# Kernel tuning notes

Measured on AMD Instinct MI355X. Metric: run time of the kernel, lower is better.

The kernel has to match this reference:

```python
import jax, jax.numpy as jnp
import numpy as np

N_NODES = 100000
N_EDGES = 1600000
N_GRAPHS = 64
FEAT = 64
EMB = 64
HID = 64
VOCAB = 32


def setup_inputs() -> dict:
    key = jax.random.key(0)
    ks = jax.random.split(key, 20)
    w = lambda k, sh: (jax.random.normal(k, sh, jnp.float32) * 0.05)
    x = jax.random.normal(ks[0], (N_NODES, FEAT), jnp.float32)
    edge_index = jax.random.randint(ks[1], (2, N_EDGES), 0, N_NODES, dtype=jnp.int32).astype(jnp.int64)
    batch = jnp.sort(jax.random.randint(ks[2], (N_NODES,), 0, N_GRAPHS, dtype=jnp.int32)).astype(jnp.int64)
    return {
        'x': x, 'edge_index': edge_index, 'batch': batch,
        # RGCN layer 1 (single relation): relation weight, root weight, bias
        'W1': w(ks[3], (FEAT, EMB)), 'root1': w(ks[4], (FEAT, EMB)), 'b1': w(ks[5], (EMB,)),
        # RGCN layer 2
        'W2': w(ks[6], (EMB, HID)), 'root2': w(ks[7], (EMB, HID)), 'b2': w(ks[8], (HID,)),
        # init_h / init_c linear heads
        'Wh': w(ks[9], (HID, HID)), 'bh': w(ks[10], (HID,)),
        'Wc': w(ks[11], (HID, HID)), 'bc': w(ks[12], (HID,)),
        # output layer
        'Wo': w(ks[13], (HID, VOCAB)), 'bo': w(ks[14], (VOCAB,)),
    }


def _rgcn(x, edge_index, W, root, b):
    # PyG RGCNConv with num_relations=1, aggr='mean':
    # out[i] = mean_{j in N(i)} (x[j] @ W) + x[i] @ root + b
    src, dst = edge_index[0], edge_index[1]
    msg = x[src] @ W                                    # [E, out] gather + small GEMM
    agg = jax.ops.segment_sum(msg, dst, num_segments=x.shape[0])
    cnt = jax.ops.segment_sum(jnp.ones((edge_index.shape[1],), x.dtype), dst, num_segments=x.shape[0])
    agg = agg / jnp.maximum(cnt, 1.0)[:, None]
    return agg + x @ root + b


def reference(x, edge_index, batch, W1, root1, b1, W2, root2, b2, Wh, bh, Wc, bc, Wo, bo):
    h = jax.nn.relu(_rgcn(x, edge_index, W1, root1, b1))
    h = jax.nn.relu(_rgcn(h, edge_index, W2, root2, b2))
    # global_mean_pool over graph-assignment vector `batch`
    summ = jax.ops.segment_sum(h, batch, num_segments=N_GRAPHS)
    cnt = jax.ops.segment_sum(jnp.ones((h.shape[0],), h.dtype), batch, num_segments=N_GRAPHS)
    pooled = summ / jnp.maximum(cnt, 1.0)[:, None]      # [G, HID]
    hidden = pooled @ Wh + bh
    cell = pooled @ Wc + bc
    logits = jax.nn.log_softmax(hidden @ Wo + bo, axis=1)
    return (logits, hidden, cell)
```

## Files before the change

kernel.cpp:

```cpp
#include <hip/hip_runtime.h>
#include <hip/hip_bf16.h>


typedef __attribute__((ext_vector_type(8))) short short8;
typedef __attribute__((ext_vector_type(4))) float f32x4;
typedef __attribute__((ext_vector_type(2))) float f32x2;

#define RB 9
#define MAXBINS 256
#define CAP 12288
#define BCAP 14336
#define CHUNK 8192

__device__ inline float bf2f(unsigned short h) {
    return __uint_as_float(((unsigned int)h) << 16);
}
__device__ inline float bflo(unsigned int u) { return __uint_as_float(u << 16); }
__device__ inline float bfhi(unsigned int u) { return __uint_as_float(u & 0xffff0000u); }
__device__ inline unsigned short f2bf(float f) {
    unsigned int u = __float_as_uint(f);
    u = (u + 0x7fffu + ((u >> 16) & 1u)) >> 16;
    return (unsigned short)u;
}

__global__ __launch_bounds__(256) void bin_prep(const int* __restrict__ src,
                                                const int* __restrict__ dst,
                                                unsigned int* __restrict__ coarse,
                                                int* __restrict__ gcur,
                                                int E, int BINS, int nbBin,
                                                const float* __restrict__ W1,
                                                const float* __restrict__ R1,
                                                const float* __restrict__ W2,
                                                const float* __restrict__ R2,
                                                unsigned short* __restrict__ bt) {
    __shared__ int cnt[MAXBINS];
    __shared__ int incl[MAXBINS];
    __shared__ int bstart[MAXBINS];
    __shared__ int bcur[MAXBINS];
    __shared__ int gbase[MAXBINS];
    __shared__ unsigned int stage[CHUNK];
    __shared__ unsigned char binOf[CHUNK];

    const int tid = threadIdx.x;
    if (blockIdx.x >= nbBin) {
        const int layer = blockIdx.x - nbBin;
        const float* W = layer ? W2 : W1;
        const float* R = layer ? R2 : R1;
        unsigned short* o = bt + (size_t)layer * 8192;
        for (int idx = tid; idx < 8192; idx += 256) {
            const int n = idx >> 6, k = idx & 63;
            const float v = (n < 64) ? W[k * 64 + n] : R[k * 64 + (n - 64)];
            o[idx] = f2bf(v);
        }
        return;
    }

    const int chunk0 = blockIdx.x * CHUNK;
    int myS[32], myD[32];
#pragma unroll
    for (int k = 0; k < 32; ++k) {
        const int idx = chunk0 + k * 256 + tid;
        if (idx < E) { myS[k] = src[idx]; myD[k] = dst[idx]; }
        else myD[k] = -1;
    }
    cnt[tid] = 0;
    __syncthreads();
#pragma unroll
    for (int k = 0; k < 32; ++k)
        if (myD[k] >= 0) atomicAdd(&cnt[myD[k] >> RB], 1);
    __syncthreads();
    incl[tid] = cnt[tid];
    __syncthreads();
    for (int off = 1; off < 256; off <<= 1) {
        int t = (tid >= off) ? incl[tid - off] : 0;
        __syncthreads();
        incl[tid] += t;
        __syncthreads();
    }
    bstart[tid] = incl[tid] - cnt[tid];
    bcur[tid] = incl[tid] - cnt[tid];
    __syncthreads();
#pragma unroll
    for (int k = 0; k < 32; ++k) {
        if (myD[k] >= 0) {
            const int b = myD[k] >> RB;
            const int pos = atomicAdd(&bcur[b], 1);
            stage[pos] = (unsigned int)myS[k] | ((unsigned int)(myD[k] & ((1 << RB) - 1)) << 17);
            binOf[pos] = (unsigned char)b;
        }
    }
    __syncthreads();
    if (tid < BINS && cnt[tid] > 0)
        gbase[tid] = tid * CAP + atomicAdd(&gcur[tid], cnt[tid]);
    __syncthreads();
    int total = E - chunk0;
    if (total > CHUNK) total = CHUNK;
    for (int idx = tid; idx < total; idx += 256) {
        const int b = binOf[idx];
        coarse[gbase[b] + (idx - bstart[b])] = stage[idx];
    }
}

__device__ inline void store_xw_fp8(unsigned char* __restrict__ xw8, int rowbase, int q,
                                    int t, int mm, const f32x4& accT) {
#pragma unroll
    for (int r = 0; r < 4; ++r) {
        const float v0 = accT[r];
        const float v1 = __shfl_down(v0, 1);
        const float v2 = __shfl_down(v0, 2);
        const float v3 = __shfl_down(v0, 3);
        if (!(mm & 3)) {
            unsigned int u = (unsigned int)__builtin_amdgcn_cvt_pk_fp8_f32(v0, v1, 0, false);
            u = (unsigned int)__builtin_amdgcn_cvt_pk_fp8_f32(v2, v3, (int)u, true);
            *(unsigned int*)&xw8[(size_t)(rowbase + q * 4 + r) * 64 + t * 16 + mm] = u;
        }
    }
}

__global__ __launch_bounds__(256) void fin_gemm1(const unsigned int* __restrict__ coarse,
                                                 const int* __restrict__ gcur,
                                                 int* __restrict__ bucket,
                                                 int* __restrict__ pstart,
                                                 int* __restrict__ degarr,
                                                 int N, int BINS,
                                                 const float* __restrict__ x,
                                                 const unsigned short* __restrict__ bt,
                                                 const float* __restrict__ bias,
                                                 unsigned char* __restrict__ xw8,
                                                 unsigned short* __restrict__ xrb) {
    __shared__ int ncnt[512];
    __shared__ int pexcl[512];
    __shared__ int ncur[512];
    __shared__ int s2[256];
    __shared__ int ptot;

    const int tid = threadIdx.x;
    if (blockIdx.x < (unsigned)BINS) {
        const int b = blockIdx.x;
        const int cb = gcur[b];
        const int base = b * BCAP;
        const unsigned int* reg = coarse + (size_t)b * CAP;
        const int node0 = b << RB;
        int nloc = N - node0;
        if (nloc > 512) nloc = 512;

        ncnt[tid] = 0; ncnt[tid + 256] = 0;
        __syncthreads();
        for (int idx = tid; idx < cb; idx += 256)
            atomicAdd(&ncnt[reg[idx] >> 17], 1);
        __syncthreads();
        const int p0 = (ncnt[2 * tid] + 15) & ~15;
        const int p1 = (ncnt[2 * tid + 1] + 15) & ~15;
        s2[tid] = p0 + p1;
        __syncthreads();
        for (int off = 1; off < 256; off <<= 1) {
            int t = (tid >= off) ? s2[tid - off] : 0;
            __syncthreads();
            s2[tid] += t;
            __syncthreads();
        }
        const int pairExcl = s2[tid] - (p0 + p1);
        pexcl[2 * tid] = pairExcl;
        pexcl[2 * tid + 1] = pairExcl + p0;
        ncur[2 * tid] = pairExcl;
        ncur[2 * tid + 1] = pairExcl + p0;
        if (tid == 255) ptot = s2[255];
        __syncthreads();
        const int total = ptot;
        for (int i = tid; i < nloc; i += 256) {
            pstart[node0 + i] = base + pexcl[i];
            degarr[node0 + i] = ncnt[i];
        }
        for (int idx = tid; idx < total; idx += 256) bucket[base + idx] = N;
        __syncthreads();
        for (int idx = tid; idx < cb; idx += 256) {
            const unsigned int e = reg[idx];
            const int p = atomicAdd(&ncur[e >> 17], 1);
            bucket[base + p] = (int)(e & 0x1FFFFu);
        }
        return;
    }

    const int gb = blockIdx.x - BINS;
    if (gb == 0 && tid < 16)
        *(unsigned int*)&xw8[(size_t)N * 64 + tid * 4] = 0u;

    const int lane = tid & 63;
    const int q = lane >> 4;
    const int mm = lane & 15;

    short8 bfrag[8][2];
#pragma unroll
    for (int t = 0; t < 8; ++t)
#pragma unroll
        for (int c = 0; c < 2; ++c)
            bfrag[t][c] = *(const short8*)&bt[(size_t)(t * 16 + mm) * 64 + c * 32 + q * 8];
    float bv[4];
#pragma unroll
    for (int tt = 0; tt < 4; ++tt) bv[tt] = bias[tt * 16 + mm];

    const int wid = tid >> 6;
    const int gw = gb * 4 + wid;
    const int nw = 1024 * 4;
    const int ntiles = N >> 4;

    for (int tile = gw; tile < ntiles; tile += nw) {
        const int row0 = tile << 4;
        const float* ap = &x[(size_t)(row0 + mm) * 64 + q * 8];
        const float4 f0 = *(const float4*)ap;
        const float4 f1 = *(const float4*)(ap + 4);
        const float4 f2 = *(const float4*)(ap + 32);
        const float4 f3 = *(const float4*)(ap + 36);
        short8 a0, a1;
        a0[0] = (short)f2bf(f0.x); a0[1] = (short)f2bf(f0.y);
        a0[2] = (short)f2bf(f0.z); a0[3] = (short)f2bf(f0.w);
        a0[4] = (short)f2bf(f1.x); a0[5] = (short)f2bf(f1.y);
        a0[6] = (short)f2bf(f1.z); a0[7] = (short)f2bf(f1.w);
        a1[0] = (short)f2bf(f2.x); a1[1] = (short)f2bf(f2.y);
        a1[2] = (short)f2bf(f2.z); a1[3] = (short)f2bf(f2.w);
        a1[4] = (short)f2bf(f3.x); a1[5] = (short)f2bf(f3.y);
        a1[6] = (short)f2bf(f3.z); a1[7] = (short)f2bf(f3.w);
        f32x4 acc[8];
#pragma unroll
        for (int t = 0; t < 8; ++t) {
            acc[t] = (f32x4){0.f, 0.f, 0.f, 0.f};
            acc[t] = __builtin_amdgcn_mfma_f32_16x16x32_bf16(a0, bfrag[t][0], acc[t], 0, 0, 0);
            acc[t] = __builtin_amdgcn_mfma_f32_16x16x32_bf16(a1, bfrag[t][1], acc[t], 0, 0, 0);
        }
#pragma unroll
        for (int t = 0; t < 4; ++t) store_xw_fp8(xw8, row0, q, t, mm, acc[t]);
#pragma unroll
        for (int t = 4; t < 8; ++t) {
#pragma unroll
            for (int r = 0; r < 4; ++r) {
                const float v = acc[t][r] + bv[t - 4];
                const float vn = __shfl_down(v, 1);
                if (!(mm & 1)) {
                    const unsigned int u = (unsigned int)f2bf(v) | ((unsigned int)f2bf(vn) << 16);
                    *(unsigned int*)&xrb[(size_t)(row0 + q * 4 + r) * 64 + (t - 4) * 16 + mm] = u;
                }
            }
        }
    }
}

__global__ __launch_bounds__(256) void gemm_xwr(const unsigned short* __restrict__ xin,
                                                const unsigned short* __restrict__ bt,
                                                const float* __restrict__ bias,
                                                unsigned char* __restrict__ xw8,
                                                unsigned short* __restrict__ xrb,
                                                int M) {
    if (blockIdx.x == 0 && threadIdx.x < 16)
        *(unsigned int*)&xw8[(size_t)M * 64 + threadIdx.x * 4] = 0u;

    const int lane = threadIdx.x & 63;
    const int q = lane >> 4;
    const int mm = lane & 15;

    short8 bfrag[8][2];
#pragma unroll
    for (int t = 0; t < 8; ++t)
#pragma unroll
        for (int c = 0; c < 2; ++c)
            bfrag[t][c] = *(const short8*)&bt[(size_t)(t * 16 + mm) * 64 + c * 32 + q * 8];
    float bv[4];
#pragma unroll
    for (int tt = 0; tt < 4; ++tt) bv[tt] = bias[tt * 16 + mm];

    const int wid = threadIdx.x >> 6;
    const int gw = blockIdx.x * 4 + wid;
    const int nw = gridDim.x * 4;
    const int ntiles = M >> 4;

    for (int tile = gw; tile < ntiles; tile += nw) {
        const int row0 = tile << 4;
        const short8 a0 = *(const short8*)&xin[(size_t)(row0 + mm) * 64 + q * 8];
        const short8 a1 = *(const short8*)&xin[(size_t)(row0 + mm) * 64 + 32 + q * 8];
        f32x4 acc[8];
#pragma unroll
        for (int t = 0; t < 8; ++t) {
            acc[t] = (f32x4){0.f, 0.f, 0.f, 0.f};
            acc[t] = __builtin_amdgcn_mfma_f32_16x16x32_bf16(a0, bfrag[t][0], acc[t], 0, 0, 0);
            acc[t] = __builtin_amdgcn_mfma_f32_16x16x32_bf16(a1, bfrag[t][1], acc[t], 0, 0, 0);
        }
#pragma unroll
        for (int t = 0; t < 4; ++t) store_xw_fp8(xw8, row0, q, t, mm, acc[t]);
#pragma unroll
        for (int t = 4; t < 8; ++t) {
#pragma unroll
            for (int r = 0; r < 4; ++r) {
                const float v = acc[t][r] + bv[t - 4];
                const float vn = __shfl_down(v, 1);
                if (!(mm & 1)) {
                    const unsigned int u = (unsigned int)f2bf(v) | ((unsigned int)f2bf(vn) << 16);
                    *(unsigned int*)&xrb[(size_t)(row0 + q * 4 + r) * 64 + (t - 4) * 16 + mm] = u;
                }
            }
        }
    }
}

__global__ __launch_bounds__(256) void aggregate(const unsigned char* __restrict__ xw8,
                                                 const unsigned short* __restrict__ xrb,
                                                 const int* __restrict__ pstart,
                                                 const int* __restrict__ degarr,
                                                 const int* __restrict__ bucket,
                                                 unsigned short* __restrict__ outb,
                                                 int N) {
    const int lane = threadIdx.x & 63;
    const int quarter = lane >> 4;
    const int fl = lane & 15;
    const int wid = threadIdx.x >> 6;
    const int gw = blockIdx.x * 4 + wid;
    const int nw = gridDim.x * 4;

    for (int i = gw; i < N; i += nw) {
        const int r0 = pstart[i];
        const int dg = degarr[i];
        const int pdeg = (dg + 15) & ~15;
        float a0 = 0.f, a1 = 0.f, a2 = 0.f, a3 = 0.f;
        for (int base = 0; base < pdeg; base += 64) {
            const int rem = pdeg - base;
            const int s = (lane < rem) ? bucket[r0 + base + lane] : N;
            const int mm = rem < 64 ? rem : 64;
            for (int t = 0; t < mm; t += 16) {
                unsigned int u[4];
#pragma unroll
                for (int p = 0; p < 4; ++p) {
                    const int rr = __shfl(s, t + 4 * p + quarter);
                    u[p] = *(const unsigned int*)&xw8[(size_t)rr * 64 + fl * 4];
                }
#pragma unroll
                for (int p = 0; p < 4; ++p) {
                    const f32x2 lo = __builtin_amdgcn_cvt_pk_f32_fp8(u[p], false);
                    const f32x2 hi = __builtin_amdgcn_cvt_pk_f32_fp8(u[p], true);
                    a0 += lo.x; a1 += lo.y; a2 += hi.x; a3 += hi.y;
                }
            }
        }
        a0 += __shfl_xor(a0, 16); a1 += __shfl_xor(a1, 16);
        a2 += __shfl_xor(a2, 16); a3 += __shfl_xor(a3, 16);
        a0 += __shfl_xor(a0, 32); a1 += __shfl_xor(a1, 32);
        a2 += __shfl_xor(a2, 32); a3 += __shfl_xor(a3, 32);

        const float inv = 1.0f / (float)(dg > 0 ? dg : 1);
        if (quarter == 0) {
            const uint2 ur = *(const uint2*)&xrb[(size_t)i * 64 + fl * 4];
            const float o0 = fmaxf(a0 * inv + bflo(ur.x), 0.f);
            const float o1 = fmaxf(a1 * inv + bfhi(ur.x), 0.f);
            const float o2 = fmaxf(a2 * inv + bflo(ur.y), 0.f);
            const float o3 = fmaxf(a3 * inv + bfhi(ur.y), 0.f);
            uint2 w;
            w.x = (unsigned int)f2bf(o0) | ((unsigned int)f2bf(o1) << 16);
            w.y = (unsigned int)f2bf(o2) | ((unsigned int)f2bf(o3) << 16);
            *(uint2*)&outb[(size_t)i * 64 + fl * 4] = w;
        }
    }
}

__global__ __launch_bounds__(256) void pool_kernel(const unsigned short* __restrict__ h,
                                                   const int* __restrict__ batch,
                                                   float* __restrict__ pooled, int N) {
    __shared__ float red[16][64];
    __shared__ int bnds[2];
    const int gph = blockIdx.x;
    if (threadIdx.x < 2) {
        const int target = gph + threadIdx.x;
        int lo = 0, hi = N;
        while (lo < hi) {
            int mid = (lo + hi) >> 1;
            if (batch[mid] < target) lo = mid + 1; else hi = mid;
        }
        bnds[threadIdx.x] = lo;
    }
    __syncthreads();
    const int r0 = bnds[0], r1 = bnds[1];
    const int f = threadIdx.x & 15;
    const int r = threadIdx.x >> 4;
    float4 acc = {0.f, 0.f, 0.f, 0.f};
    for (int row = r0 + r; row < r1; row += 16) {
        const ushort4 v = *(const ushort4*)&h[(size_t)row * 64 + f * 4];
        acc.x += bf2f(v.x); acc.y += bf2f(v.y);
        acc.z += bf2f(v.z); acc.w += bf2f(v.w);
    }
    red[r][f * 4 + 0] = acc.x; red[r][f * 4 + 1] = acc.y;
    red[r][f * 4 + 2] = acc.z; red[r][f * 4 + 3] = acc.w;
    __syncthreads();
    if (threadIdx.x < 64) {
        float s = 0.f;
        for (int j = 0; j < 16; ++j) s += red[j][threadIdx.x];
        const int cnt = r1 - r0;
        const float invc = 1.0f / (float)(cnt > 0 ? cnt : 1);
        pooled[gph * 64 + threadIdx.x] = s * invc;
    }
}

__global__ __launch_bounds__(256) void head_kernel(const float* __restrict__ pooled,
                                                   const float* __restrict__ Wh,
                                                   const float* __restrict__ bh,
                                                   const float* __restrict__ Wc,
                                                   const float* __restrict__ bc,
                                                   const float* __restrict__ Wo,
                                                   const float* __restrict__ bo,
                                                   float* __restrict__ out) {
    __shared__ float pm[4096];
    __shared__ float hid[4096];
    __shared__ float lg[2048];
    const int t = threadIdx.x;

    for (int idx = t; idx < 4096; idx += 256) pm[idx] = pooled[idx];
    __syncthreads();

    for (int idx = t; idx < 4096; idx += 256) {
        int g = idx >> 6, o = idx & 63;
        float ah = bh[o], ac = bc[o];
        for (int k = 0; k < 64; ++k) {
            float p = pm[(g << 6) + k];
            ah += p * Wh[k * 64 + o];
            ac += p * Wc[k * 64 + o];
        }
        hid[idx] = ah;
        out[2048 + idx] = ah;
        out[6144 + idx] = ac;
    }
    __syncthreads();

    for (int idx = t; idx < 2048; idx += 256) {
        int g = idx >> 5, v = idx & 31;
        float a = bo[v];
        for (int k = 0; k < 64; ++k) a += hid[(g << 6) + k] * Wo[k * 32 + v];
        lg[idx] = a;
    }
    __syncthreads();

    if (t < 64) {
        float mx = -3.4e38f;
        for (int v = 0; v < 32; ++v) mx = fmaxf(mx, lg[(t << 5) + v]);
        float s = 0.f;
        for (int v = 0; v < 32; ++v) s += expf(lg[(t << 5) + v] - mx);
        float lse = mx + logf(s);
        for (int v = 0; v < 32; ++v) out[(t << 5) + v] = lg[(t << 5) + v] - lse;
    }
}

extern "C" void kernel_launch(void* const* d_in, const int* in_sizes, int n_in,
                              void* d_out, int out_size, void* d_ws, size_t ws_size,
                              hipStream_t stream) {
    const float* x = (const float*)d_in[0];
    const int* ei = (const int*)d_in[1];
    const int* batch = (const int*)d_in[2];
    const float* W1 = (const float*)d_in[3];
    const float* root1 = (const float*)d_in[4];
    const float* b1 = (const float*)d_in[5];
    const float* W2 = (const float*)d_in[6];
    const float* root2 = (const float*)d_in[7];
    const float* b2 = (const float*)d_in[8];
    const float* Wh = (const float*)d_in[9];
    const float* bh = (const float*)d_in[10];
    const float* Wc = (const float*)d_in[11];
    const float* bc = (const float*)d_in[12];
    const float* Wo = (const float*)d_in[13];
    const float* bo = (const float*)d_in[14];
    float* out = (float*)d_out;

    const int N = in_sizes[0] / 64;
    const int E = in_sizes[1] / 2;
    const int* srcp = ei;
    const int* dstp = ei + E;
    const int BINS = (N + (1 << RB) - 1) >> RB;

    char* ws = (char*)d_ws;
    size_t off = 0;
    auto alloc = [&](size_t bytes) -> void* {
        void* p = ws + off;
        off += (bytes + 255) & ~(size_t)255;
        return p;
    };
    int* pstart = (int*)alloc((size_t)N * 4);
    int* degarr = (int*)alloc((size_t)N * 4);
    int* bucket = (int*)alloc(((size_t)BINS * BCAP + 256) * 4);
    unsigned int* coarse = (unsigned int*)alloc((size_t)BINS * CAP * 4);
    unsigned short* h1 = (unsigned short*)alloc((size_t)N * 64 * 2);
    unsigned short* h2 = (unsigned short*)alloc((size_t)N * 64 * 2);
    unsigned char* xw8 = (unsigned char*)alloc((size_t)(N + 1) * 64);
    unsigned short* xrb = (unsigned short*)alloc((size_t)N * 64 * 2);
    unsigned short* bt = (unsigned short*)alloc(2 * 8192 * 2);
    float* pooled = (float*)alloc(4096 * 4);
    int* gcur = (int*)alloc(MAXBINS * 4);

    const int nbBin = (E + CHUNK - 1) / CHUNK;

    hipMemsetAsync(gcur, 0, MAXBINS * 4, stream);
    bin_prep<<<nbBin + 2, 256, 0, stream>>>(srcp, dstp, coarse, gcur, E, BINS, nbBin,
                                            W1, root1, W2, root2, bt);
    fin_gemm1<<<BINS + 1024, 256, 0, stream>>>(coarse, gcur, bucket, pstart, degarr, N, BINS,
                                               x, bt, b1, xw8, xrb);
    aggregate<<<4096, 256, 0, stream>>>(xw8, xrb, pstart, degarr, bucket, h1, N);
    gemm_xwr<<<1024, 256, 0, stream>>>(h1, bt + 8192, b2, xw8, xrb, N);
    aggregate<<<4096, 256, 0, stream>>>(xw8, xrb, pstart, degarr, bucket, h2, N);

    pool_kernel<<<64, 256, 0, stream>>>(h2, batch, pooled, N);
    head_kernel<<<1, 256, 0, stream>>>(pooled, Wh, bh, Wc, bc, Wo, bo, out);
}
```

Baseline: 282.2 us.

## Fuse layer-1 GEMM into edge binning kernel and build weight fragments in-register

Moves the layer-1 x@[W1|root1] MFMA GEMM out of the CSR-finalize kernel and into the edge-binning kernel, so the GEMM blocks run alongside the binning blocks instead of after them. Each GEMM wave now reads the fp32 weights directly and converts them to bf16 fragments in registers, which removes the separate transposed-weight buffer. Separate xw8/xrb buffers are allocated for layer 2, and the fp8 store gains a row bound check. The trade-off is more strided scalar weight loads per wave and a kernel with heavier register and shared-memory use.

```diff
diff --git a/kernel.cpp b/kernel.cpp
--- a/kernel.cpp
+++ b/kernel.cpp
@@ -23,16 +23,53 @@
     return (unsigned short)u;
 }
 
-__global__ __launch_bounds__(256) void bin_prep(const int* __restrict__ src,
-                                                const int* __restrict__ dst,
-                                                unsigned int* __restrict__ coarse,
-                                                int* __restrict__ gcur,
-                                                int E, int BINS, int nbBin,
-                                                const float* __restrict__ W1,
-                                                const float* __restrict__ R1,
-                                                const float* __restrict__ W2,
-                                                const float* __restrict__ R2,
-                                                unsigned short* __restrict__ bt) {
+__device__ inline void build_bfrag(const float* __restrict__ W,
+                                   const float* __restrict__ R,
+                                   int q, int mm, short8 bfrag[8][2]) {
+#pragma unroll
+    for (int t = 0; t < 8; ++t) {
+        const int n = t * 16 + mm;
+        const float* P = (n < 64) ? (W + n) : (R + n - 64);
+#pragma unroll
+        for (int c = 0; c < 2; ++c) {
+#pragma unroll
+            for (int j = 0; j < 8; ++j) {
+                const int k = c * 32 + q * 8 + j;
+                bfrag[t][c][j] = (short)f2bf(P[k * 64]);
+            }
+        }
+    }
+}
+
+__device__ inline void store_xw_fp8(unsigned char* __restrict__ xw8, int rowbase, int q,
+                                    int t, int mm, const f32x4& accT, int N) {
+#pragma unroll
+    for (int r = 0; r < 4; ++r) {
+        const float v0 = accT[r];
+        const float v1 = __shfl_down(v0, 1);
+        const float v2 = __shfl_down(v0, 2);
+        const float v3 = __shfl_down(v0, 3);
+        const int orow = rowbase + q * 4 + r;
+        if (!(mm & 3) && orow < N) {
+            unsigned int u = (unsigned int)__builtin_amdgcn_cvt_pk_fp8_f32(v0, v1, 0, false);
+            u = (unsigned int)__builtin_amdgcn_cvt_pk_fp8_f32(v2, v3, (int)u, true);
+            *(unsigned int*)&xw8[(size_t)orow * 64 + t * 16 + mm] = u;
+        }
+    }
+}
+
+__global__ __launch_bounds__(256) void bin_gemm1(const int* __restrict__ src,
+                                                 const int* __restrict__ dst,
+                                                 unsigned int* __restrict__ coarse,
+                                                 int* __restrict__ gcur,
+                                                 int E, int BINS, int nbBin,
+                                                 const float* __restrict__ x,
+                                                 const float* __restrict__ W1,
+                                                 const float* __restrict__ R1,
+                                                 const float* __restrict__ bias,
+                                                 unsigned char* __restrict__ xw8,
+                                                 unsigned short* __restrict__ xrb,
+                                                 int N) {
     __shared__ int cnt[MAXBINS];
     __shared__ int incl[MAXBINS];
     __shared__ int bstart[MAXBINS];
@@ -42,15 +79,63 @@
     __shared__ unsigned char binOf[CHUNK];
 
     const int tid = threadIdx.x;
-    if (blockIdx.x >= nbBin) {
-        const int layer = blockIdx.x - nbBin;
-        const float* W = layer ? W2 : W1;
-        const float* R = layer ? R2 : R1;
-        unsigned short* o = bt + (size_t)layer * 8192;
-        for (int idx = tid; idx < 8192; idx += 256) {
-            const int n = idx >> 6, k = idx & 63;
-            const float v = (n < 64) ? W[k * 64 + n] : R[k * 64 + (n - 64)];
-            o[idx] = f2bf(v);
+    if (blockIdx.x >= (unsigned)nbBin) {
+        const int gb = blockIdx.x - nbBin;
+        if (gb == 0 && tid < 16)
+            *(unsigned int*)&xw8[(size_t)N * 64 + tid * 4] = 0u;
+
+        const int lane = tid & 63;
+        const int q = lane >> 4;
+        const int mm = lane & 15;
+
+        short8 bfrag[8][2];
+        build_bfrag(W1, R1, q, mm, bfrag);
+        float bv[4];
+#pragma unroll
+        for (int tt = 0; tt < 4; ++tt) bv[tt] = bias[tt * 16 + mm];
+
+        const int wid = tid >> 6;
+        const int gw = gb * 4 + wid;
+        const int nw = 1024 * 4;
+        const int ntiles = N >> 4;
+
+        for (int tile = gw; tile < ntiles; tile += nw) {
+            const int row0 = tile << 4;
+            const float* ap = &x[(size_t)(row0 + mm) * 64 + q * 8];
+            const float4 f0 = *(const float4*)ap;
+            const float4 f1 = *(const float4*)(ap + 4);
+            const float4 f2 = *(const float4*)(ap + 32);
+            const float4 f3 = *(const float4*)(ap + 36);
+            short8 a0, a1;
+            a0[0] = (short)f2bf(f0.x); a0[1] = (short)f2bf(f0.y);
+            a0[2] = (short)f2bf(f0.z); a0[3] = (short)f2bf(f0.w);
+            a0[4] = (short)f2bf(f1.x); a0[5] = (short)f2bf(f1.y);
+            a0[6] = (short)f2bf(f1.z); a0[7] = (short)f2bf(f1.w);
+            a1[0] = (short)f2bf(f2.x); a1[1] = (short)f2bf(f2.y);
+            a1[2] = (short)f2bf(f2.z); a1[3] = (short)f2bf(f2.w);
+            a1[4] = (short)f2bf(f3.x); a1[5] = (short)f2bf(f3.y);
+            a1[6] = (short)f2bf(f3.z); a1[7] = (short)f2bf(f3.w);
+            f32x4 acc[8];
+#pragma unroll
+            for (int t = 0; t < 8; ++t) {
+                acc[t] = (f32x4){0.f, 0.f, 0.f, 0.f};
+                acc[t] = __builtin_amdgcn_mfma_f32_16x16x32_bf16(a0, bfrag[t][0], acc[t], 0, 0, 0);
+                acc[t] = __builtin_amdgcn_mfma_f32_16x16x32_bf16(a1, bfrag[t][1], acc[t], 0, 0, 0);
+            }
+#pragma unroll
+            for (int t = 0; t < 4; ++t) store_xw_fp8(xw8, row0, q, t, mm, acc[t], N);
+#pragma unroll
+            for (int t = 4; t < 8; ++t) {
+#pragma unroll
+                for (int r = 0; r < 4; ++r) {
+                    const float v = acc[t][r] + bv[t - 4];
+                    const float vn = __shfl_down(v, 1);
+                    if (!(mm & 1)) {
+                        const unsigned int u = (unsigned int)f2bf(v) | ((unsigned int)f2bf(vn) << 16);
+                        *(unsigned int*)&xrb[(size_t)(row0 + q * 4 + r) * 64 + (t - 4) * 16 + mm] = u;
+                    }
+                }
+            }
         }
         return;
     }
@@ -101,202 +186,58 @@
     }
 }
 
-__device__ inline void store_xw_fp8(unsigned char* __restrict__ xw8, int rowbase, int q,
-                                    int t, int mm, const f32x4& accT) {
-#pragma unroll
-    for (int r = 0; r < 4; ++r) {
-        const float v0 = accT[r];
-        const float v1 = __shfl_down(v0, 1);
-        const float v2 = __shfl_down(v0, 2);
-        const float v3 = __shfl_down(v0, 3);
-        if (!(mm & 3)) {
-            unsigned int u = (unsigned int)__builtin_amdgcn_cvt_pk_fp8_f32(v0, v1, 0, false);
-            u = (unsigned int)__builtin_amdgcn_cvt_pk_fp8_f32(v2, v3, (int)u, true);
-            *(unsigned int*)&xw8[(size_t)(rowbase + q * 4 + r) * 64 + t * 16 + mm] = u;
-        }
-    }
-}
-
-__global__ __launch_bounds__(256) void fin_gemm1(const unsigned int* __restrict__ coarse,
-                                                 const int* __restrict__ gcur,
-                                                 int* __restrict__ bucket,
-                                                 int* __restrict__ pstart,
-                                                 int* __restrict__ degarr,
-                                                 int N, int BINS,
-                                                 const float* __restrict__ x,
-                                                 const unsigned short* __restrict__ bt,
-                                                 const float* __restrict__ bias,
-                                                 unsigned char* __restrict__ xw8,
-                                                 unsigned short* __restrict__ xrb) {
+__global__ __launch_bounds__(256) void finalize_csr(const unsigned int* __restrict__ coarse,
+                                                    const int* __restrict__ gcur,
+                                                    int* __restrict__ bucket,
+                                                    int* __restrict__ pstart,
+                                                    int* __restrict__ degarr,
+                                                    int N, int BINS) {
     __shared__ int ncnt[512];
     __shared__ int pexcl[512];
     __shared__ int ncur[512];
     __shared__ int s2[256];
-    __shared__ int ptot;
 
     const int tid = threadIdx.x;
-    if (blockIdx.x < (unsigned)BINS) {
-        const int b = blockIdx.x;
-        const int cb = gcur[b];
-        const int base = b * BCAP;
-        const unsigned int* reg = coarse + (size_t)b * CAP;
-        const int node0 = b << RB;
-        int nloc = N - node0;
-        if (nloc > 512) nloc = 512;
-
-        ncnt[tid] = 0; ncnt[tid + 256] = 0;
+    const int b = blockIdx.x;
+    const int cb = gcur[b];
+    const int base = b * BCAP;
+    const unsigned int* reg = coarse + (size_t)b * CAP;
+    const int node0 = b << RB;
+    int nloc = N - node0;
+    if (nloc > 512) nloc = 512;
+
+    ncnt[tid] = 0; ncnt[tid + 256] = 0;
+    __syncthreads();
+    for (int idx = tid; idx < cb; idx += 256)
+        atomicAdd(&ncnt[reg[idx] >> 17], 1);
+    __syncthreads();
+    const int p0 = (ncnt[2 * tid] + 15) & ~15;
+    const int p1 = (ncnt[2 * tid + 1] + 15) & ~15;
+    s2[tid] = p0 + p1;
+    __syncthreads();
+    for (int off = 1; off < 256; off <<= 1) {
+        int t = (tid >= off) ? s2[tid - off] : 0;
         __syncthreads();
-        for (int idx = tid; idx < cb; idx += 256)
-            atomicAdd(&ncnt[reg[idx] >> 17], 1);
+        s2[tid] += t;
         __syncthreads();
-        const int p0 = (ncnt[2 * tid] + 15) & ~15;
-        const int p1 = (ncnt[2 * tid + 1] + 15) & ~15;
-        s2[tid] = p0 + p1;
-        __syncthreads();
-        for (int off = 1; off < 256; off <<= 1) {
-            int t = (tid >= off) ? s2[tid - off] : 0;
-            __syncthreads();
-            s2[tid] += t;
-            __syncthreads();
-        }
-        const int pairExcl = s2[tid] - (p0 + p1);
-        pexcl[2 * tid] = pairExcl;
-        pexcl[2 * tid + 1] = pairExcl + p0;
-        ncur[2 * tid] = pairExcl;
-        ncur[2 * tid + 1] = pairExcl + p0;
-        if (tid == 255) ptot = s2[255];
-        __syncthreads();
-        const int total = ptot;
-        for (int i = tid; i < nloc; i += 256) {
-            pstart[node0 + i] = base + pexcl[i];
-            degarr[node0 + i] = ncnt[i];
-        }
-        for (int idx = tid; idx < total; idx += 256) bucket[base + idx] = N;
-        __syncthreads();
-        for (int idx = tid; idx < cb; idx += 256) {
-            const unsigned int e = reg[idx];
-            const int p = atomicAdd(&ncur[e >> 17], 1);
-            bucket[base + p] = (int)(e & 0x1FFFFu);
-        }
-        return;
-    }
-
-    const int gb = blockIdx.x - BINS;
-    if (gb == 0 && tid < 16)
-        *(unsigned int*)&xw8[(size_t)N * 64 + tid * 4] = 0u;
-
-    const int lane = tid & 63;
-    const int q = lane >> 4;
-    const int mm = lane & 15;
-
-    short8 bfrag[8][2];
-#pragma unroll
-    for (int t = 0; t < 8; ++t)
-#pragma unroll
-        for (int c = 0; c < 2; ++c)
-            bfrag[t][c] = *(const short8*)&bt[(size_t)(t * 16 + mm) * 64 + c * 32 + q * 8];
-    float bv[4];
-#pragma unroll
-    for (int tt = 0; tt < 4; ++tt) bv[tt] = bias[tt * 16 + mm];
-
-    const int wid = tid >> 6;
-    const int gw = gb * 4 + wid;
-    const int nw = 1024 * 4;
-    const int ntiles = N >> 4;
-
-    for (int tile = gw; tile < ntiles; tile += nw) {
-        const int row0 = tile << 4;
-        const float* ap = &x[(size_t)(row0 + mm) * 64 + q * 8];
-        const float4 f0 = *(const float4*)ap;
-        const float4 f1 = *(const float4*)(ap + 4);
-        const float4 f2 = *(const float4*)(ap + 32);
-        const float4 f3 = *(const float4*)(ap + 36);
-        short8 a0, a1;
-        a0[0] = (short)f2bf(f0.x); a0[1] = (short)f2bf(f0.y);
-        a0[2] = (short)f2bf(f0.z); a0[3] = (short)f2bf(f0.w);
-        a0[4] = (short)f2bf(f1.x); a0[5] = (short)f2bf(f1.y);
-        a0[6] = (short)f2bf(f1.z); a0[7] = (short)f2bf(f1.w);
-        a1[0] = (short)f2bf(f2.x); a1[1] = (short)f2bf(f2.y);
-        a1[2] = (short)f2bf(f2.z); a1[3] = (short)f2bf(f2.w);
-        a1[4] = (short)f2bf(f3.x); a1[5] = (short)f2bf(f3.y);
-        a1[6] = (short)f2bf(f3.z); a1[7] = (short)f2bf(f3.w);
-        f32x4 acc[8];
-#pragma unroll
-        for (int t = 0; t < 8; ++t) {
-            acc[t] = (f32x4){0.f, 0.f, 0.f, 0.f};
-            acc[t] = __builtin_amdgcn_mfma_f32_16x16x32_bf16(a0, bfrag[t][0], acc[t], 0, 0, 0);
-            acc[t] = __builtin_amdgcn_mfma_f32_16x16x32_bf16(a1, bfrag[t][1], acc[t], 0, 0, 0);
-        }
-#pragma unroll
-        for (int t = 0; t < 4; ++t) store_xw_fp8(xw8, row0, q, t, mm, acc[t]);
-#pragma unroll
-        for (int t = 4; t < 8; ++t) {
-#pragma unroll
-            for (int r = 0; r < 4; ++r) {
-                const float v = acc[t][r] + bv[t - 4];
-                const float vn = __shfl_down(v, 1);
-                if (!(mm & 1)) {
-                    const unsigned int u = (unsigned int)f2bf(v) | ((unsigned int)f2bf(vn) << 16);
-                    *(unsigned int*)&xrb[(size_t)(row0 + q * 4 + r) * 64 + (t - 4) * 16 + mm] = u;
-                }
-            }
-        }
-    }
-}
-
-__global__ __launch_bounds__(256) void gemm_xwr(const unsigned short* __restrict__ xin,
-                                                const unsigned short* __restrict__ bt,
-                                                const float* __restrict__ bias,
-                                                unsigned char* __restrict__ xw8,
-                                                unsigned short* __restrict__ xrb,
-                                                int M) {
-    if (blockIdx.x == 0 && threadIdx.x < 16)
-        *(unsigned int*)&xw8[(size_t)M * 64 + threadIdx.x * 4] = 0u;
-
-    const int lane = threadIdx.x & 63;
-    const int q = lane >> 4;
-    const int mm = lane & 15;
-
-    short8 bfrag[8][2];
-#pragma unroll
-    for (int t = 0; t < 8; ++t)
-#pragma unroll
-        for (int c = 0; c < 2; ++c)
-            bfrag[t][c] = *(const short8*)&bt[(size_t)(t * 16 + mm) * 64 + c * 32 + q * 8];
-    float bv[4];
-#pragma unroll
-    for (int tt = 0; tt < 4; ++tt) bv[tt] = bias[tt * 16 + mm];
-
-    const int wid = threadIdx.x >> 6;
-    const int gw = blockIdx.x * 4 + wid;
-    const int nw = gridDim.x * 4;
-    const int ntiles = M >> 4;
-
-    for (int tile = gw; tile < ntiles; tile += nw) {
-        const int row0 = tile << 4;
-        const short8 a0 = *(const short8*)&xin[(size_t)(row0 + mm) * 64 + q * 8];
-        const short8 a1 = *(const short8*)&xin[(size_t)(row0 + mm) * 64 + 32 + q * 8];
-        f32x4 acc[8];
-#pragma unroll
-        for (int t = 0; t < 8; ++t) {
-            acc[t] = (f32x4){0.f, 0.f, 0.f, 0.f};
-            acc[t] = __builtin_amdgcn_mfma_f32_16x16x32_bf16(a0, bfrag[t][0], acc[t], 0, 0, 0);
-            acc[t] = __builtin_amdgcn_mfma_f32_16x16x32_bf16(a1, bfrag[t][1], acc[t], 0, 0, 0);
-        }
-#pragma unroll
-        for (int t = 0; t < 4; ++t) store_xw_fp8(xw8, row0, q, t, mm, acc[t]);
-#pragma unroll
-        for (int t = 4; t < 8; ++t) {
-#pragma unroll
-            for (int r = 0; r < 4; ++r) {
-                const float v = acc[t][r] + bv[t - 4];
-                const float vn = __shfl_down(v, 1);
-                if (!(mm & 1)) {
-                    const unsigned int u = (unsigned int)f2bf(v) | ((unsigned int)f2bf(vn) << 16);
-                    *(unsigned int*)&xrb[(size_t)(row0 + q * 4 + r) * 64 + (t - 4) * 16 + mm] = u;
-                }
-            }
-        }
+    }
+    const int pairExcl = s2[tid] - (p0 + p1);
+    pexcl[2 * tid] = pairExcl;
+    pexcl[2 * tid + 1] = pairExcl + p0;
+    ncur[2 * tid] = pairExcl;
+    ncur[2 * tid + 1] = pairExcl + p0;
+    __syncthreads();
+    const int total = s2[255];
+    for (int i = tid; i < nloc; i += 256) {
+        pstart[node0 + i] = base + pexcl[i];
+        degarr[node0 + i] = ncnt[i];
+    }
+    for (int idx = tid; idx < total; idx += 256) bucket[base + idx] = N;
+    __syncthreads();
+    for (int idx = tid; idx < cb; idx += 256) {
+        const unsigned int e = reg[idx];
+        const int p = atomicAdd(&ncur[e >> 17], 1);
+        bucket[base + p] = (int)(e & 0x1FFFFu);
     }
 }
 
@@ -354,6 +295,59 @@
             w.x = (unsigned int)f2bf(o0) | ((unsigned int)f2bf(o1) << 16);
             w.y = (unsigned int)f2bf(o2) | ((unsigned int)f2bf(o3) << 16);
             *(uint2*)&outb[(size_t)i * 64 + fl * 4] = w;
+        }
+    }
+}
+
+__global__ __launch_bounds__(256) void gemm_xwr2(const unsigned short* __restrict__ xin,
+                                                 const float* __restrict__ W2,
+                                                 const float* __restrict__ R2,
+                                                 const float* __restrict__ bias,
+                                                 unsigned char* __restrict__ xw8,
+                                                 unsigned short* __restrict__ xrb,
+                                                 int M) {
+    if (blockIdx.x == 0 && threadIdx.x < 16)
+        *(unsigned int*)&xw8[(size_t)M * 64 + threadIdx.x * 4] = 0u;
+
+    const int lane = threadIdx.x & 63;
+    const int q = lane >> 4;
+    const int mm = lane & 15;
+
+    short8 bfrag[8][2];
+    build_bfrag(W2, R2, q, mm, bfrag);
+    float bv[4];
+#pragma unroll
+    for (int tt = 0; tt < 4; ++tt) bv[tt] = bias[tt * 16 + mm];
+
+    const int wid = threadIdx.x >> 6;
+    const int gw = blockIdx.x * 4 + wid;
+    const int nw = gridDim.x * 4;
+    const int ntiles = M >> 4;
+
+    for (int tile = gw; tile < ntiles; tile += nw) {
+        const int row0 = tile << 4;
+        const short8 a0 = *(const short8*)&xin[(size_t)(row0 + mm) * 64 + q * 8];
+        const short8 a1 = *(const short8*)&xin[(size_t)(row0 + mm) * 64 + 32 + q * 8];
+        f32x4 acc[8];
+#pragma unroll
+        for (int t = 0; t < 8; ++t) {
+            acc[t] = (f32x4){0.f, 0.f, 0.f, 0.f};
+            acc[t] = __builtin_amdgcn_mfma_f32_16x16x32_bf16(a0, bfrag[t][0], acc[t], 0, 0, 0);
+            acc[t] = __builtin_amdgcn_mfma_f32_16x16x32_bf16(a1, bfrag[t][1], acc[t], 0, 0, 0);
+        }
+#pragma unroll
+        for (int t = 0; t < 4; ++t) store_xw_fp8(xw8, row0, q, t, mm, acc[t], M);
+#pragma unroll
+        for (int t = 4; t < 8; ++t) {
+#pragma unroll
+            for (int r = 0; r < 4; ++r) {
+                const float v = acc[t][r] + bv[t - 4];
+                const float vn = __shfl_down(v, 1);
+                if (!(mm & 1)) {
+                    const unsigned int u = (unsigned int)f2bf(v) | ((unsigned int)f2bf(vn) << 16);
+                    *(unsigned int*)&xrb[(size_t)(row0 + q * 4 + r) * 64 + (t - 4) * 16 + mm] = u;
+                }
+            }
         }
     }
 }
@@ -483,22 +477,21 @@
     unsigned short* h1 = (unsigned short*)alloc((size_t)N * 64 * 2);
     unsigned short* h2 = (unsigned short*)alloc((size_t)N * 64 * 2);
     unsigned char* xw8 = (unsigned char*)alloc((size_t)(N + 1) * 64);
+    unsigned char* xw8b = (unsigned char*)alloc((size_t)(N + 1) * 64);
     unsigned short* xrb = (unsigned short*)alloc((size_t)N * 64 * 2);
-    unsigned short* bt = (unsigned short*)alloc(2 * 8192 * 2);
+    unsigned short* xrb2 = (unsigned short*)alloc((size_t)N * 64 * 2);
     float* pooled = (float*)alloc(4096 * 4);
     int* gcur = (int*)alloc(MAXBINS * 4);
 
     const int nbBin = (E + CHUNK - 1) / CHUNK;
 
     hipMemsetAsync(gcur, 0, MAXBINS * 4, stream);
-    bin_prep<<<nbBin + 2, 256, 0, stream>>>(srcp, dstp, coarse, gcur, E, BINS, nbBin,
-                                            W1, root1, W2, root2, bt);
-    fin_gemm1<<<BINS + 1024, 256, 0, stream>>>(coarse, gcur, bucket, pstart, degarr, N, BINS,
-                                               x, bt, b1, xw8, xrb);
+    bin_gemm1<<<nbBin + 1024, 256, 0, stream>>>(srcp, dstp, coarse, gcur, E, BINS, nbBin,
+                                                x, W1, root1, b1, xw8, xrb, N);
+    finalize_csr<<<BINS, 256, 0, stream>>>(coarse, gcur, bucket, pstart, degarr, N, BINS);
     aggregate<<<4096, 256, 0, stream>>>(xw8, xrb, pstart, degarr, bucket, h1, N);
-    gemm_xwr<<<1024, 256, 0, stream>>>(h1, bt + 8192, b2, xw8, xrb, N);
-    aggregate<<<4096, 256, 0, stream>>>(xw8, xrb, pstart, degarr, bucket, h2, N);
-
+    gemm_xwr2<<<1024, 256, 0, stream>>>(h1, W2, root2, b2, xw8b, xrb2, N);
+    aggregate<<<4096, 256, 0, stream>>>(xw8b, xrb2, pstart, degarr, bucket, h2, N);
     pool_kernel<<<64, 256, 0, stream>>>(h2, batch, pooled, N);
     head_kernel<<<1, 256, 0, stream>>>(pooled, Wh, bh, Wc, bc, Wo, bo, out);
 }
```

After: 282.8 us. About the same (+0.2%).
